# Optimization experiments

Hardware: AMD Instinct MI355X
Metric: run time of the kernel (lower is better)

Reference implementation:

```python
import jax, jax.numpy as jnp
import numpy as np

N_TOKEN = 267735
D_EMBED = 1024
D_PROJ = 1024
CUTOFF_ENDS = [0, 20000, 40000, 200000, N_TOKEN]
DIV_VAL = 4
INIT_STD = 0.02


def setup_inputs() -> dict:
    key = jax.random.key(0)
    ks = jax.random.split(key, 9)
    inp = jax.random.randint(ks[0], (8, 4096), 0, N_TOKEN, dtype=jnp.int64)
    out = {"inp": inp}
    for i in range(4):
        l, r = CUTOFF_ENDS[i], CUTOFF_ENDS[i + 1]
        d_emb_i = D_EMBED // (DIV_VAL ** i)
        out[f"emb{i}"] = jax.random.normal(ks[1 + i], (r - l, d_emb_i), dtype=jnp.float32) * INIT_STD
        out[f"proj{i}"] = jax.random.normal(ks[5 + i], (d_emb_i, D_PROJ), dtype=jnp.float32) * INIT_STD
    return out


def reference(inp, emb0, emb1, emb2, emb3, proj0, proj1, proj2, proj3):
    embs = [emb0, emb1, emb2, emb3]
    projs = [proj0, proj1, proj2, proj3]
    flat = inp.reshape(-1)  # [N]
    out = jnp.zeros((flat.shape[0], D_PROJ), dtype=jnp.float32)
    for i in range(4):
        l, r = CUTOFF_ENDS[i], CUTOFF_ENDS[i + 1]
        mask = (flat >= l) & (flat < r)  # [N]
        idx = jnp.clip(flat - l, 0, r - l - 1)  # in-range even for out-of-bucket tokens
        e = embs[i][idx]                         # [N, d_emb_i] gather
        p = jnp.einsum('id,de->ie', e, projs[i])  # [N, D_PROJ]
        out = out + jnp.where(mask[:, None], p, 0.0)
    emb_scale = D_PROJ ** 0.5
    return (out * emb_scale).reshape(inp.shape + (D_PROJ,))
```

## Files before the change

kernel.cpp:

```cpp
#include <hip/hip_runtime.h>
#include <hip/hip_bf16.h>

#define N_TOK   32768
#define DPROJ   1024
#define SCALE   32.0f

typedef short bf16x8 __attribute__((ext_vector_type(8)));
typedef float f32x4  __attribute__((ext_vector_type(4)));

__device__ __forceinline__ short f2bf(float f) {
    unsigned u = __builtin_bit_cast(unsigned, f);
    unsigned r = (u + 0x7FFFu + ((u >> 16) & 1u)) >> 16;
    return (short)r;
}

__global__ void k_prep(const int* __restrict__ inp, int* __restrict__ cnt,
                       int* __restrict__ perm, int* __restrict__ rowidx,
                       const float* __restrict__ p0, const float* __restrict__ p1,
                       const float* __restrict__ p2, const float* __restrict__ p3,
                       short* __restrict__ t0, short* __restrict__ t1,
                       short* __restrict__ t2, short* __restrict__ t3)
{
    __shared__ float tile[128][17];

    if (blockIdx.x < 128) {
        int i = blockIdx.x * 256 + threadIdx.x;
        int t = inp[i];
        int b, l;
        if (t < 20000)       { b = 0; l = 0; }
        else if (t < 40000)  { b = 1; l = 20000; }
        else if (t < 200000) { b = 2; l = 40000; }
        else                 { b = 3; l = 200000; }

        unsigned long long m0 = __ballot(b == 0);
        unsigned long long m1 = __ballot(b == 1);
        unsigned long long m2 = __ballot(b == 2);
        unsigned long long m3 = __ballot(b == 3);

        int lane = threadIdx.x & 63;
        int mybase = 0;
        if (lane < 4) {
            unsigned long long mm = (lane == 0) ? m0 : (lane == 1) ? m1 : (lane == 2) ? m2 : m3;
            mybase = atomicAdd(&cnt[lane], __popcll(mm));
        }
        int base = __shfl(mybase, b);
        unsigned long long mine = (b == 0) ? m0 : (b == 1) ? m1 : (b == 2) ? m2 : m3;
        unsigned long long lt = (lane == 0) ? 0ull : (~0ull >> (64 - lane));
        int pos = base + __popcll(mine & lt);
        perm[b * N_TOK + pos]   = i;
        rowidx[b * N_TOK + pos] = t - l;
        return;
    }

    int bid = blockIdx.x - 128;
    const float* src; short* dst; int K; int rel;
    if (bid < 512)      { src = p0; dst = t0; K = 1024; rel = bid; }
    else if (bid < 640) { src = p1; dst = t1; K = 256;  rel = bid - 512; }
    else if (bid < 704) { src = p2; dst = t2; K = 64;   rel = bid - 640; }
    else                { src = p3; dst = t3; K = 16;   rel = bid - 704; }
    int ktiles = (K + 127) >> 7;
    int k0 = (rel % ktiles) * 128;
    int n0 = (rel / ktiles) * 16;
    int t = threadIdx.x;

    #pragma unroll
    for (int i = 0; i < 2; ++i) {
        int idx = t + i * 256;
        int k = idx >> 2;
        int nc = (idx & 3) * 4;
        if (k0 + k < K) {
            float4 v = *reinterpret_cast<const float4*>(src + (size_t)(k0 + k) * DPROJ + n0 + nc);
            tile[k][nc + 0] = v.x; tile[k][nc + 1] = v.y;
            tile[k][nc + 2] = v.z; tile[k][nc + 3] = v.w;
        }
    }
    __syncthreads();
    int n  = t >> 4;
    int kc = (t & 15) * 8;
    if (k0 + kc < K) {
        short s[8];
        #pragma unroll
        for (int j = 0; j < 8; ++j) s[j] = f2bf(tile[kc + j][n]);
        *reinterpret_cast<int4*>(dst + (size_t)(n0 + n) * K + k0 + kc) =
            *reinterpret_cast<const int4*>(s);
    }
}

__global__ __launch_bounds__(256, 2) void k_gemm(
    const float* __restrict__ e0, const float* __restrict__ e1,
    const float* __restrict__ e2, const float* __restrict__ e3,
    const short* __restrict__ t0, const short* __restrict__ t1,
    const short* __restrict__ t2, const short* __restrict__ t3,
    const int* __restrict__ cnt, const int* __restrict__ perm,
    const int* __restrict__ rowidx, float* __restrict__ out)
{
    __shared__ short As[64][40];
    __shared__ short Bs[256][40];

    const int c0 = cnt[0], c1 = cnt[1], c2 = cnt[2], c3 = cnt[3];
    const int q0 = (c0 + 63) & ~63;
    const int q1 = q0 + ((c1 + 63) & ~63);
    const int q2 = q1 + ((c2 + 63) & ~63);
    const int q3 = q2 + ((c3 + 63) & ~63);
    const int p0 = blockIdx.y * 64;
    if (p0 >= q3) return;
    int b, M, m0, K; const float* emb; const short* bt;
    if (p0 < q0)      { b = 0; M = c0; m0 = p0;      K = 1024; emb = e0; bt = t0; }
    else if (p0 < q1) { b = 1; M = c1; m0 = p0 - q0; K = 256;  emb = e1; bt = t1; }
    else if (p0 < q2) { b = 2; M = c2; m0 = p0 - q1; K = 64;   emb = e2; bt = t2; }
    else              { b = 3; M = c3; m0 = p0 - q2; K = 16;   emb = e3; bt = t3; }
    if (m0 >= M) return;
    const int* pperm = perm   + b * N_TOK;
    const int* prow  = rowidx + b * N_TOK;

    const int tid  = threadIdx.x;
    const int lane = tid & 63;
    const int w    = tid >> 6;
    const int n0   = blockIdx.x * 256;

    const int ar = tid >> 2;
    const int ac = (tid & 3) * 8;
    const bool avalid = (m0 + ar) < M;
    const int  arow   = avalid ? prow[m0 + ar] : 0;
    const float* aptr = emb + (size_t)arow * K;

    f32x4 acc[4][4];
    #pragma unroll
    for (int mi = 0; mi < 4; ++mi)
        #pragma unroll
        for (int ni = 0; ni < 4; ++ni) acc[mi][ni] = (f32x4)0.0f;

    const int koff = (lane >> 4) * 8;
    const int fr   = lane & 15;

    for (int k0 = 0; k0 < K; k0 += 32) {
        float av[8];
        #pragma unroll
        for (int j = 0; j < 8; ++j) av[j] = 0.0f;
        if (avalid && (k0 + ac) < K) {
            float4 x = *reinterpret_cast<const float4*>(aptr + k0 + ac);
            float4 y = *reinterpret_cast<const float4*>(aptr + k0 + ac + 4);
            av[0] = x.x; av[1] = x.y; av[2] = x.z; av[3] = x.w;
            av[4] = y.x; av[5] = y.y; av[6] = y.z; av[7] = y.w;
        }
        short bv[4][8];
        #pragma unroll
        for (int g = 0; g < 4; ++g) {
            int bn = g * 64 + (tid >> 2);
            int bq = (tid & 3) * 8;
            if ((k0 + bq) < K) {
                *reinterpret_cast<int4*>(&bv[g][0]) =
                    *reinterpret_cast<const int4*>(bt + (size_t)(n0 + bn) * K + k0 + bq);
            } else {
                #pragma unroll
                for (int j = 0; j < 8; ++j) bv[g][j] = 0;
            }
        }
        __syncthreads();
        {
            short asv[8];
            #pragma unroll
            for (int j = 0; j < 8; ++j) asv[j] = f2bf(av[j]);
            *reinterpret_cast<int4*>(&As[ar][ac]) = *reinterpret_cast<const int4*>(asv);
            #pragma unroll
            for (int g = 0; g < 4; ++g)
                *reinterpret_cast<int4*>(&Bs[g * 64 + (tid >> 2)][(tid & 3) * 8]) =
                    *reinterpret_cast<const int4*>(&bv[g][0]);
        }
        __syncthreads();

        bf16x8 afr[4], bfr[4];
        #pragma unroll
        for (int mi = 0; mi < 4; ++mi)
            afr[mi] = *reinterpret_cast<const bf16x8*>(&As[mi * 16 + fr][koff]);
        #pragma unroll
        for (int ni = 0; ni < 4; ++ni)
            bfr[ni] = *reinterpret_cast<const bf16x8*>(&Bs[w * 64 + ni * 16 + fr][koff]);
        #pragma unroll
        for (int mi = 0; mi < 4; ++mi)
            #pragma unroll
            for (int ni = 0; ni < 4; ++ni)
                acc[mi][ni] = __builtin_amdgcn_mfma_f32_16x16x32_bf16(
                    afr[mi], bfr[ni], acc[mi][ni], 0, 0, 0);
    }

    const int colb = n0 + w * 64 + fr;
    const int rowg = (lane >> 4) * 4;
    #pragma unroll
    for (int mi = 0; mi < 4; ++mi) {
        #pragma unroll
        for (int j = 0; j < 4; ++j) {
            int m = m0 + mi * 16 + rowg + j;
            if (m < M) {
                size_t r = (size_t)pperm[m] * DPROJ + colb;
                out[r]      = acc[mi][0][j] * SCALE;
                out[r + 16] = acc[mi][1][j] * SCALE;
                out[r + 32] = acc[mi][2][j] * SCALE;
                out[r + 48] = acc[mi][3][j] * SCALE;
            }
        }
    }
}

__global__ void k_naive(const int* __restrict__ inp,
                        const float* __restrict__ emb0, const float* __restrict__ emb1,
                        const float* __restrict__ emb2, const float* __restrict__ emb3,
                        const float* __restrict__ proj0, const float* __restrict__ proj1,
                        const float* __restrict__ proj2, const float* __restrict__ proj3,
                        float* __restrict__ out)
{
    __shared__ float e[1024];
    int t = inp[blockIdx.x];
    const float* emb; const float* proj; int K, l;
    if (t < 20000)       { emb = emb0; proj = proj0; K = 1024; l = 0; }
    else if (t < 40000)  { emb = emb1; proj = proj1; K = 256;  l = 20000; }
    else if (t < 200000) { emb = emb2; proj = proj2; K = 64;   l = 40000; }
    else                 { emb = emb3; proj = proj3; K = 16;   l = 200000; }
    int tid = threadIdx.x;
    for (int k = tid; k < K; k += 256) e[k] = emb[(size_t)(t - l) * K + k];
    __syncthreads();
    float acc[4] = {0.f, 0.f, 0.f, 0.f};
    for (int k = 0; k < K; ++k) {
        float ek = e[k];
        #pragma unroll
        for (int c = 0; c < 4; ++c)
            acc[c] = fmaf(ek, proj[(size_t)k * DPROJ + tid + 256 * c], acc[c]);
    }
    #pragma unroll
    for (int c = 0; c < 4; ++c)
        out[(size_t)blockIdx.x * DPROJ + tid + 256 * c] = acc[c] * SCALE;
}

extern "C" void kernel_launch(void* const* d_in, const int* in_sizes, int n_in,
                              void* d_out, int out_size, void* d_ws, size_t ws_size,
                              hipStream_t stream) {
    const int*   inp   = (const int*)d_in[0];
    const float* emb0  = (const float*)d_in[1];
    const float* proj0 = (const float*)d_in[2];
    const float* emb1  = (const float*)d_in[3];
    const float* proj1 = (const float*)d_in[4];
    const float* emb2  = (const float*)d_in[5];
    const float* proj2 = (const float*)d_in[6];
    const float* emb3  = (const float*)d_in[7];
    const float* proj3 = (const float*)d_in[8];
    float* out = (float*)d_out;

    const size_t off_cnt  = 0;
    const size_t off_perm = 256;
    const size_t off_row  = off_perm + 4ull * N_TOK * 4;
    const size_t off_t0   = off_row  + 4ull * N_TOK * 4;
    const size_t off_t1   = off_t0 + 1024ull * 1024 * 2;
    const size_t off_t2   = off_t1 + 1024ull * 256 * 2;
    const size_t off_t3   = off_t2 + 1024ull * 64 * 2;
    const size_t needed   = off_t3 + 1024ull * 16 * 2;

    if (d_ws == nullptr || ws_size < needed) {
        k_naive<<<N_TOK, 256, 0, stream>>>(inp, emb0, emb1, emb2, emb3,
                                           proj0, proj1, proj2, proj3, out);
        return;
    }

    char* ws = (char*)d_ws;
    int*   cnt    = (int*)(ws + off_cnt);
    int*   perm   = (int*)(ws + off_perm);
    int*   rowidx = (int*)(ws + off_row);
    short* t0     = (short*)(ws + off_t0);
    short* t1     = (short*)(ws + off_t1);
    short* t2     = (short*)(ws + off_t2);
    short* t3     = (short*)(ws + off_t3);

    hipMemsetAsync(cnt, 0, 16, stream);
    k_prep<<<896, 256, 0, stream>>>(inp, cnt, perm, rowidx,
                                    proj0, proj1, proj2, proj3, t0, t1, t2, t3);

    dim3 grid(4, 516);
    k_gemm<<<grid, 256, 0, stream>>>(emb0, emb1, emb2, emb3,
                                     t0, t1, t2, t3,
                                     cnt, perm, rowidx, out);
}
```

Before: 62.82 us.

## Pre-gather embedding rows into compact bf16 buffers before the GEMM

Splits the prep kernel into a bucketize kernel and a second kernel. The second kernel converts the projections and also gathers each bucket's embedding rows into contiguous bf16 workspace buffers. The GEMM then loads A tiles directly as bf16 from these buffers, with no per-column-block random fp32 gather and conversion, and raises launch bounds to 3 blocks per CU. This removes the fourfold redundant gather and conversion of A. In exchange it adds a kernel launch and a write-then-read round trip of the gathered data. Rows past M in the last tile read uninitialized workspace, which is harmless only if those rows are masked at store.

```diff
diff --git a/kernel.cpp b/kernel.cpp
--- a/kernel.cpp
+++ b/kernel.cpp
@@ -4,6 +4,7 @@
 #define N_TOK   32768
 #define DPROJ   1024
 #define SCALE   32.0f
+#define MAXROWS 32832ull
 
 typedef short bf16x8 __attribute__((ext_vector_type(8)));
 typedef float f32x4  __attribute__((ext_vector_type(4)));
@@ -14,85 +15,128 @@
     return (short)r;
 }
 
-__global__ void k_prep(const int* __restrict__ inp, int* __restrict__ cnt,
-                       int* __restrict__ perm, int* __restrict__ rowidx,
-                       const float* __restrict__ p0, const float* __restrict__ p1,
-                       const float* __restrict__ p2, const float* __restrict__ p3,
-                       short* __restrict__ t0, short* __restrict__ t1,
-                       short* __restrict__ t2, short* __restrict__ t3)
+__global__ void k_bucketize(const int* __restrict__ inp, int* __restrict__ cnt,
+                            int* __restrict__ perm, int* __restrict__ rowidx) {
+    int i = blockIdx.x * 256 + threadIdx.x;
+    int t = inp[i];
+    int b, l;
+    if (t < 20000)       { b = 0; l = 0; }
+    else if (t < 40000)  { b = 1; l = 20000; }
+    else if (t < 200000) { b = 2; l = 40000; }
+    else                 { b = 3; l = 200000; }
+
+    unsigned long long m0 = __ballot(b == 0);
+    unsigned long long m1 = __ballot(b == 1);
+    unsigned long long m2 = __ballot(b == 2);
+    unsigned long long m3 = __ballot(b == 3);
+
+    int lane = threadIdx.x & 63;
+    int mybase = 0;
+    if (lane < 4) {
+        unsigned long long mm = (lane == 0) ? m0 : (lane == 1) ? m1 : (lane == 2) ? m2 : m3;
+        mybase = atomicAdd(&cnt[lane], __popcll(mm));
+    }
+    int base = __shfl(mybase, b);
+    unsigned long long mine = (b == 0) ? m0 : (b == 1) ? m1 : (b == 2) ? m2 : m3;
+    unsigned long long lt = (lane == 0) ? 0ull : (~0ull >> (64 - lane));
+    int pos = base + __popcll(mine & lt);
+    perm[b * N_TOK + pos]   = i;
+    rowidx[b * N_TOK + pos] = t - l;
+}
+
+__global__ void k_prep2(const int* __restrict__ cnt,
+                        const int* __restrict__ rowidx,
+                        const float* __restrict__ p0, const float* __restrict__ p1,
+                        const float* __restrict__ p2, const float* __restrict__ p3,
+                        short* __restrict__ t0, short* __restrict__ t1,
+                        short* __restrict__ t2, short* __restrict__ t3,
+                        const float* __restrict__ e0, const float* __restrict__ e1,
+                        const float* __restrict__ e2, const float* __restrict__ e3,
+                        short* __restrict__ ga0, short* __restrict__ ga1,
+                        short* __restrict__ ga2, short* __restrict__ ga3)
 {
     __shared__ float tile[128][17];
 
-    if (blockIdx.x < 128) {
-        int i = blockIdx.x * 256 + threadIdx.x;
-        int t = inp[i];
-        int b, l;
-        if (t < 20000)       { b = 0; l = 0; }
-        else if (t < 40000)  { b = 1; l = 20000; }
-        else if (t < 200000) { b = 2; l = 40000; }
-        else                 { b = 3; l = 200000; }
-
-        unsigned long long m0 = __ballot(b == 0);
-        unsigned long long m1 = __ballot(b == 1);
-        unsigned long long m2 = __ballot(b == 2);
-        unsigned long long m3 = __ballot(b == 3);
-
-        int lane = threadIdx.x & 63;
-        int mybase = 0;
-        if (lane < 4) {
-            unsigned long long mm = (lane == 0) ? m0 : (lane == 1) ? m1 : (lane == 2) ? m2 : m3;
-            mybase = atomicAdd(&cnt[lane], __popcll(mm));
-        }
-        int base = __shfl(mybase, b);
-        unsigned long long mine = (b == 0) ? m0 : (b == 1) ? m1 : (b == 2) ? m2 : m3;
-        unsigned long long lt = (lane == 0) ? 0ull : (~0ull >> (64 - lane));
-        int pos = base + __popcll(mine & lt);
-        perm[b * N_TOK + pos]   = i;
-        rowidx[b * N_TOK + pos] = t - l;
+    if (blockIdx.x < 768) {
+        int bid = blockIdx.x;
+        const float* src; short* dst; int K; int rel;
+        if (bid < 512)      { src = p0; dst = t0; K = 1024; rel = bid; }
+        else if (bid < 640) { src = p1; dst = t1; K = 256;  rel = bid - 512; }
+        else if (bid < 704) { src = p2; dst = t2; K = 64;   rel = bid - 640; }
+        else                { src = p3; dst = t3; K = 16;   rel = bid - 704; }
+        int ktiles = (K + 127) >> 7;
+        int k0 = (rel % ktiles) * 128;
+        int n0 = (rel / ktiles) * 16;
+        int t = threadIdx.x;
+
+        #pragma unroll
+        for (int i = 0; i < 2; ++i) {
+            int idx = t + i * 256;
+            int k = idx >> 2;
+            int nc = (idx & 3) * 4;
+            if (k0 + k < K) {
+                float4 v = *reinterpret_cast<const float4*>(src + (size_t)(k0 + k) * DPROJ + n0 + nc);
+                tile[k][nc + 0] = v.x; tile[k][nc + 1] = v.y;
+                tile[k][nc + 2] = v.z; tile[k][nc + 3] = v.w;
+            }
+        }
+        __syncthreads();
+        int n  = t >> 4;
+        int kc = (t & 15) * 8;
+        if (k0 + kc < K) {
+            short s[8];
+            #pragma unroll
+            for (int j = 0; j < 8; ++j) s[j] = f2bf(tile[kc + j][n]);
+            *reinterpret_cast<int4*>(dst + (size_t)(n0 + n) * K + k0 + kc) =
+                *reinterpret_cast<const int4*>(s);
+        }
         return;
     }
 
-    int bid = blockIdx.x - 128;
-    const float* src; short* dst; int K; int rel;
-    if (bid < 512)      { src = p0; dst = t0; K = 1024; rel = bid; }
-    else if (bid < 640) { src = p1; dst = t1; K = 256;  rel = bid - 512; }
-    else if (bid < 704) { src = p2; dst = t2; K = 64;   rel = bid - 640; }
-    else                { src = p3; dst = t3; K = 16;   rel = bid - 704; }
-    int ktiles = (K + 127) >> 7;
-    int k0 = (rel % ktiles) * 128;
-    int n0 = (rel / ktiles) * 16;
-    int t = threadIdx.x;
-
-    #pragma unroll
-    for (int i = 0; i < 2; ++i) {
-        int idx = t + i * 256;
-        int k = idx >> 2;
-        int nc = (idx & 3) * 4;
-        if (k0 + k < K) {
-            float4 v = *reinterpret_cast<const float4*>(src + (size_t)(k0 + k) * DPROJ + n0 + nc);
-            tile[k][nc + 0] = v.x; tile[k][nc + 1] = v.y;
-            tile[k][nc + 2] = v.z; tile[k][nc + 3] = v.w;
-        }
-    }
-    __syncthreads();
-    int n  = t >> 4;
-    int kc = (t & 15) * 8;
-    if (k0 + kc < K) {
-        short s[8];
-        #pragma unroll
-        for (int j = 0; j < 8; ++j) s[j] = f2bf(tile[kc + j][n]);
-        *reinterpret_cast<int4*>(dst + (size_t)(n0 + n) * K + k0 + kc) =
-            *reinterpret_cast<const int4*>(s);
-    }
-}
-
-__global__ __launch_bounds__(256, 2) void k_gemm(
-    const float* __restrict__ e0, const float* __restrict__ e1,
-    const float* __restrict__ e2, const float* __restrict__ e3,
+    int bid = blockIdx.x - 768;
+    const int c0 = cnt[0], c1 = cnt[1], c2 = cnt[2], c3 = cnt[3];
+    const int q0 = (c0 + 63) & ~63;
+    const int q1 = q0 + ((c1 + 63) & ~63);
+    const int q2 = q1 + ((c2 + 63) & ~63);
+    const int q3 = q2 + ((c3 + 63) & ~63);
+    const int p0g = bid * 64;
+    if (p0g >= q3) return;
+    int b, M, m0, K; const float* emb; short* ga;
+    if (p0g < q0)      { b = 0; M = c0; m0 = p0g;      K = 1024; emb = e0; ga = ga0; }
+    else if (p0g < q1) { b = 1; M = c1; m0 = p0g - q0; K = 256;  emb = e1; ga = ga1; }
+    else if (p0g < q2) { b = 2; M = c2; m0 = p0g - q1; K = 64;   emb = e2; ga = ga2; }
+    else               { b = 3; M = c3; m0 = p0g - q2; K = 16;   emb = e3; ga = ga3; }
+    if (m0 >= M) return;
+
+    const int tid = threadIdx.x;
+    const int r   = tid >> 2;
+    const int c   = (tid & 3) * 8;
+    const int gm  = m0 + r;
+    if (gm >= M) return;
+    const int arow = rowidx[b * N_TOK + gm];
+    const float* src = emb + (size_t)arow * K;
+    short* dst = ga + (size_t)gm * K;
+
+    for (int k0 = 0; k0 < K; k0 += 32) {
+        int col = k0 + c;
+        if (col < K) {
+            float4 x = *reinterpret_cast<const float4*>(src + col);
+            float4 y = *reinterpret_cast<const float4*>(src + col + 4);
+            short s[8];
+            s[0] = f2bf(x.x); s[1] = f2bf(x.y); s[2] = f2bf(x.z); s[3] = f2bf(x.w);
+            s[4] = f2bf(y.x); s[5] = f2bf(y.y); s[6] = f2bf(y.z); s[7] = f2bf(y.w);
+            *reinterpret_cast<int4*>(dst + col) = *reinterpret_cast<const int4*>(s);
+        }
+    }
+}
+
+__global__ __launch_bounds__(256, 3) void k_gemm(
+    const short* __restrict__ ga0, const short* __restrict__ ga1,
+    const short* __restrict__ ga2, const short* __restrict__ ga3,
     const short* __restrict__ t0, const short* __restrict__ t1,
     const short* __restrict__ t2, const short* __restrict__ t3,
     const int* __restrict__ cnt, const int* __restrict__ perm,
-    const int* __restrict__ rowidx, float* __restrict__ out)
+    float* __restrict__ out)
 {
     __shared__ short As[64][40];
     __shared__ short Bs[256][40];
@@ -104,25 +148,22 @@
     const int q3 = q2 + ((c3 + 63) & ~63);
     const int p0 = blockIdx.y * 64;
     if (p0 >= q3) return;
-    int b, M, m0, K; const float* emb; const short* bt;
-    if (p0 < q0)      { b = 0; M = c0; m0 = p0;      K = 1024; emb = e0; bt = t0; }
-    else if (p0 < q1) { b = 1; M = c1; m0 = p0 - q0; K = 256;  emb = e1; bt = t1; }
-    else if (p0 < q2) { b = 2; M = c2; m0 = p0 - q1; K = 64;   emb = e2; bt = t2; }
-    else              { b = 3; M = c3; m0 = p0 - q2; K = 16;   emb = e3; bt = t3; }
+    int b, M, m0, K; const short* ga; const short* bt;
+    if (p0 < q0)      { b = 0; M = c0; m0 = p0;      K = 1024; ga = ga0; bt = t0; }
+    else if (p0 < q1) { b = 1; M = c1; m0 = p0 - q0; K = 256;  ga = ga1; bt = t1; }
+    else if (p0 < q2) { b = 2; M = c2; m0 = p0 - q1; K = 64;   ga = ga2; bt = t2; }
+    else              { b = 3; M = c3; m0 = p0 - q2; K = 16;   ga = ga3; bt = t3; }
     if (m0 >= M) return;
-    const int* pperm = perm   + b * N_TOK;
-    const int* prow  = rowidx + b * N_TOK;
+    const int* pperm = perm + b * N_TOK;
 
     const int tid  = threadIdx.x;
     const int lane = tid & 63;
     const int w    = tid >> 6;
     const int n0   = blockIdx.x * 256;
 
-    const int ar = tid >> 2;
-    const int ac = (tid & 3) * 8;
-    const bool avalid = (m0 + ar) < M;
-    const int  arow   = avalid ? prow[m0 + ar] : 0;
-    const float* aptr = emb + (size_t)arow * K;
+    const int sr = tid >> 2;
+    const int sc = (tid & 3) * 8;
+    const short* aptr = ga + (size_t)(m0 + sr) * K;
 
     f32x4 acc[4][4];
     #pragma unroll
@@ -134,39 +175,24 @@
     const int fr   = lane & 15;
 
     for (int k0 = 0; k0 < K; k0 += 32) {
-        float av[8];
-        #pragma unroll
-        for (int j = 0; j < 8; ++j) av[j] = 0.0f;
-        if (avalid && (k0 + ac) < K) {
-            float4 x = *reinterpret_cast<const float4*>(aptr + k0 + ac);
-            float4 y = *reinterpret_cast<const float4*>(aptr + k0 + ac + 4);
-            av[0] = x.x; av[1] = x.y; av[2] = x.z; av[3] = x.w;
-            av[4] = y.x; av[5] = y.y; av[6] = y.z; av[7] = y.w;
-        }
-        short bv[4][8];
+        int4 a4 = make_int4(0, 0, 0, 0);
+        if ((k0 + sc) < K)
+            a4 = *reinterpret_cast<const int4*>(aptr + k0 + sc);
+        int4 bv[4];
         #pragma unroll
         for (int g = 0; g < 4; ++g) {
-            int bn = g * 64 + (tid >> 2);
-            int bq = (tid & 3) * 8;
-            if ((k0 + bq) < K) {
-                *reinterpret_cast<int4*>(&bv[g][0]) =
-                    *reinterpret_cast<const int4*>(bt + (size_t)(n0 + bn) * K + k0 + bq);
+            if ((k0 + sc) < K) {
+                bv[g] = *reinterpret_cast<const int4*>(
+                    bt + (size_t)(n0 + g * 64 + sr) * K + k0 + sc);
             } else {
-                #pragma unroll
-                for (int j = 0; j < 8; ++j) bv[g][j] = 0;
+                bv[g] = make_int4(0, 0, 0, 0);
             }
         }
         __syncthreads();
-        {
-            short asv[8];
-            #pragma unroll
-            for (int j = 0; j < 8; ++j) asv[j] = f2bf(av[j]);
-            *reinterpret_cast<int4*>(&As[ar][ac]) = *reinterpret_cast<const int4*>(asv);
-            #pragma unroll
-            for (int g = 0; g < 4; ++g)
-                *reinterpret_cast<int4*>(&Bs[g * 64 + (tid >> 2)][(tid & 3) * 8]) =
-                    *reinterpret_cast<const int4*>(&bv[g][0]);
-        }
+        *reinterpret_cast<int4*>(&As[sr][sc]) = a4;
+        #pragma unroll
+        for (int g = 0; g < 4; ++g)
+            *reinterpret_cast<int4*>(&Bs[g * 64 + sr][sc]) = bv[g];
         __syncthreads();
 
         bf16x8 afr[4], bfr[4];
@@ -252,7 +278,11 @@
     const size_t off_t1   = off_t0 + 1024ull * 1024 * 2;
     const size_t off_t2   = off_t1 + 1024ull * 256 * 2;
     const size_t off_t3   = off_t2 + 1024ull * 64 * 2;
-    const size_t needed   = off_t3 + 1024ull * 16 * 2;
+    const size_t off_ga0  = off_t3 + 1024ull * 16 * 2;
+    const size_t off_ga1  = off_ga0 + MAXROWS * 1024 * 2;
+    const size_t off_ga2  = off_ga1 + MAXROWS * 256 * 2;
+    const size_t off_ga3  = off_ga2 + MAXROWS * 64 * 2;
+    const size_t needed   = off_ga3 + MAXROWS * 16 * 2;
 
     if (d_ws == nullptr || ws_size < needed) {
         k_naive<<<N_TOK, 256, 0, stream>>>(inp, emb0, emb1, emb2, emb3,
@@ -268,13 +298,21 @@
     short* t1     = (short*)(ws + off_t1);
     short* t2     = (short*)(ws + off_t2);
     short* t3     = (short*)(ws + off_t3);
+    short* ga0    = (short*)(ws + off_ga0);
+    short* ga1    = (short*)(ws + off_ga1);
+    short* ga2    = (short*)(ws + off_ga2);
+    short* ga3    = (short*)(ws + off_ga3);
 
     hipMemsetAsync(cnt, 0, 16, stream);
-    k_prep<<<896, 256, 0, stream>>>(inp, cnt, perm, rowidx,
-                                    proj0, proj1, proj2, proj3, t0, t1, t2, t3);
+    k_bucketize<<<N_TOK / 256, 256, 0, stream>>>(inp, cnt, perm, rowidx);
+    k_prep2<<<768 + 516, 256, 0, stream>>>(cnt, rowidx,
+                                           proj0, proj1, proj2, proj3,
+                                           t0, t1, t2, t3,
+                                           emb0, emb1, emb2, emb3,
+                                           ga0, ga1, ga2, ga3);
 
     dim3 grid(4, 516);
-    k_gemm<<<grid, 256, 0, stream>>>(emb0, emb1, emb2, emb3,
+    k_gemm<<<grid, 256, 0, stream>>>(ga0, ga1, ga2, ga3,
                                      t0, t1, t2, t3,
-                                     cnt, perm, rowidx, out);
-}
+                                     cnt, perm, out);
+}
```

Result: slower. 72.64 us (+15.6%).

## Prefetch next K-tile into registers and swizzle block-to-tile mapping

Applied to the files above, without the earlier changes.

Global loads for the next K step are now issued right after the current tile is written to shared memory, so they overlap with the MFMA work instead of stalling at the top of each iteration. Block indices are also remapped so groups of 8 row tiles sweep all 4 column panels together, which is meant to improve L2 reuse of gathered embedding rows and projection panels. The grid grows to 520 rows so it divides evenly under the swizzle. This costs extra registers for the prefetch buffers, which may hurt occupancy under the 2-blocks-per-SM launch bound.

```diff
diff --git a/kernel.cpp b/kernel.cpp
--- a/kernel.cpp
+++ b/kernel.cpp
@@ -97,12 +97,16 @@
     __shared__ short As[64][40];
     __shared__ short Bs[256][40];
 
+    const int hw     = blockIdx.y * 4 + blockIdx.x;
+    const int ytile  = (hw >> 5) * 8 + (hw & 7);
+    const int panel  = (hw >> 3) & 3;
+
     const int c0 = cnt[0], c1 = cnt[1], c2 = cnt[2], c3 = cnt[3];
     const int q0 = (c0 + 63) & ~63;
     const int q1 = q0 + ((c1 + 63) & ~63);
     const int q2 = q1 + ((c2 + 63) & ~63);
     const int q3 = q2 + ((c3 + 63) & ~63);
-    const int p0 = blockIdx.y * 64;
+    const int p0 = ytile * 64;
     if (p0 >= q3) return;
     int b, M, m0, K; const float* emb; const short* bt;
     if (p0 < q0)      { b = 0; M = c0; m0 = p0;      K = 1024; emb = e0; bt = t0; }
@@ -116,12 +120,12 @@
     const int tid  = threadIdx.x;
     const int lane = tid & 63;
     const int w    = tid >> 6;
-    const int n0   = blockIdx.x * 256;
-
-    const int ar = tid >> 2;
-    const int ac = (tid & 3) * 8;
-    const bool avalid = (m0 + ar) < M;
-    const int  arow   = avalid ? prow[m0 + ar] : 0;
+    const int n0   = panel * 256;
+
+    const int sr = tid >> 2;
+    const int sc = (tid & 3) * 8;
+    const bool avalid = (m0 + sr) < M;
+    const int  arow   = avalid ? prow[m0 + sr] : 0;
     const float* aptr = emb + (size_t)arow * K;
 
     f32x4 acc[4][4];
@@ -133,40 +137,40 @@
     const int koff = (lane >> 4) * 8;
     const int fr   = lane & 15;
 
+    float av[8];
+    int4  bv[4];
+#define ISSUE_LOADS(K0)                                                        \
+    {                                                                          \
+        _Pragma("unroll")                                                      \
+        for (int j = 0; j < 8; ++j) av[j] = 0.0f;                              \
+        if (avalid && ((K0) + sc) < K) {                                       \
+            float4 x = *reinterpret_cast<const float4*>(aptr + (K0) + sc);     \
+            float4 y = *reinterpret_cast<const float4*>(aptr + (K0) + sc + 4); \
+            av[0] = x.x; av[1] = x.y; av[2] = x.z; av[3] = x.w;                \
+            av[4] = y.x; av[5] = y.y; av[6] = y.z; av[7] = y.w;                \
+        }                                                                      \
+        _Pragma("unroll")                                                      \
+        for (int g = 0; g < 4; ++g) {                                          \
+            if (((K0) + sc) < K)                                               \
+                bv[g] = *reinterpret_cast<const int4*>(                        \
+                    bt + (size_t)(n0 + g * 64 + sr) * K + (K0) + sc);          \
+            else bv[g] = make_int4(0, 0, 0, 0);                                \
+        }                                                                      \
+    }
+
+    ISSUE_LOADS(0);
     for (int k0 = 0; k0 < K; k0 += 32) {
-        float av[8];
-        #pragma unroll
-        for (int j = 0; j < 8; ++j) av[j] = 0.0f;
-        if (avalid && (k0 + ac) < K) {
-            float4 x = *reinterpret_cast<const float4*>(aptr + k0 + ac);
-            float4 y = *reinterpret_cast<const float4*>(aptr + k0 + ac + 4);
-            av[0] = x.x; av[1] = x.y; av[2] = x.z; av[3] = x.w;
-            av[4] = y.x; av[5] = y.y; av[6] = y.z; av[7] = y.w;
-        }
-        short bv[4][8];
-        #pragma unroll
-        for (int g = 0; g < 4; ++g) {
-            int bn = g * 64 + (tid >> 2);
-            int bq = (tid & 3) * 8;
-            if ((k0 + bq) < K) {
-                *reinterpret_cast<int4*>(&bv[g][0]) =
-                    *reinterpret_cast<const int4*>(bt + (size_t)(n0 + bn) * K + k0 + bq);
-            } else {
-                #pragma unroll
-                for (int j = 0; j < 8; ++j) bv[g][j] = 0;
-            }
-        }
         __syncthreads();
         {
             short asv[8];
             #pragma unroll
             for (int j = 0; j < 8; ++j) asv[j] = f2bf(av[j]);
-            *reinterpret_cast<int4*>(&As[ar][ac]) = *reinterpret_cast<const int4*>(asv);
+            *reinterpret_cast<int4*>(&As[sr][sc]) = *reinterpret_cast<const int4*>(asv);
             #pragma unroll
             for (int g = 0; g < 4; ++g)
-                *reinterpret_cast<int4*>(&Bs[g * 64 + (tid >> 2)][(tid & 3) * 8]) =
-                    *reinterpret_cast<const int4*>(&bv[g][0]);
-        }
+                *reinterpret_cast<int4*>(&Bs[g * 64 + sr][sc]) = bv[g];
+        }
+        if (k0 + 32 < K) ISSUE_LOADS(k0 + 32);
         __syncthreads();
 
         bf16x8 afr[4], bfr[4];
@@ -183,6 +187,7 @@
                 acc[mi][ni] = __builtin_amdgcn_mfma_f32_16x16x32_bf16(
                     afr[mi], bfr[ni], acc[mi][ni], 0, 0, 0);
     }
+#undef ISSUE_LOADS
 
     const int colb = n0 + w * 64 + fr;
     const int rowg = (lane >> 4) * 4;
@@ -273,7 +278,7 @@
     k_prep<<<896, 256, 0, stream>>>(inp, cnt, perm, rowidx,
                                     proj0, proj1, proj2, proj3, t0, t1, t2, t3);
 
-    dim3 grid(4, 516);
+    dim3 grid(4, 520);
     k_gemm<<<grid, 256, 0, stream>>>(emb0, emb1, emb2, emb3,
                                      t0, t1, t2, t3,
                                      cnt, perm, rowidx, out);
```

After: 55.82 us. 1.13x faster.
